# Kernel optimization log

Hardware: AMD Instinct MI355X
Metric: run time of the kernel (lower is better)

The kernel has to match this reference:

```python
import jax, jax.numpy as jnp
import numpy as np

N = 1048576   # total points across batch
C = 64        # in_planes
B = 16        # number of ragged segments (point clouds)
EPS = 1e-5


def setup_inputs() -> dict:
    key = jax.random.key(0)
    ks = jax.random.split(key, 4)
    x = jax.random.normal(ks[0], (N, C), dtype=jnp.float32)
    # cumulative end-offsets, strictly increasing, last == N
    rng = np.random.default_rng(0)
    w = rng.random(B) + 0.5
    ends = np.round(np.cumsum(w) / w.sum() * N).astype(np.int64)
    ends[-1] = N
    o = jnp.asarray(ends)
    # linear2: Linear(C, C) + ReLU (applied to per-segment mean)
    W2 = jax.random.normal(ks[1], (C, C), dtype=jnp.float32) / np.float32(np.sqrt(C))
    b2 = jnp.zeros((C,), jnp.float32)
    # linear1: BasicMLP(2C -> C): Linear + norm + ReLU
    W1 = jax.random.normal(ks[2], (2 * C, C), dtype=jnp.float32) / np.float32(np.sqrt(2 * C))
    b1 = jnp.zeros((C,), jnp.float32)
    gamma = jnp.ones((C,), jnp.float32)
    beta = jnp.zeros((C,), jnp.float32)
    return dict(x=x, o=o, W2=W2, b2=b2, W1=W1, b1=b1, gamma=gamma, beta=beta)


def reference(x, o, W2, b2, W1, b1, gamma, beta):
    n = x.shape[0]
    nseg = o.shape[0]
    # segment id of each point from cumulative offsets o
    seg = jnp.searchsorted(o, jnp.arange(n), side='right')          # [N]
    counts = jnp.diff(o, prepend=0).astype(x.dtype)                 # [B]
    # per-segment mean pool (x_b.sum(0) / cnt)
    sums = jax.ops.segment_sum(x, seg, num_segments=nseg)           # [B, C]
    means = sums / counts[:, None]
    # linear2: Linear + ReLU on the pooled vector
    xb = jax.nn.relu(means @ W2 + b2)                               # [B, C]
    # broadcast-repeat pooled feature back to points, concat with x
    h = jnp.concatenate([x, xb[seg]], axis=1)                       # [N, 2C]
    # linear1: Linear -> norm (LayerNorm stand-in for conditional norm) -> ReLU
    h = h @ W1 + b1                                                 # [N, C]
    mu = jnp.mean(h, axis=-1, keepdims=True)
    var = jnp.var(h, axis=-1, keepdims=True)
    h = (h - mu) * jax.lax.rsqrt(var + EPS) * gamma + beta
    return jax.nn.relu(h)
```

## Files before the change

kernel.cpp:

```cpp
#include <hip/hip_runtime.h>
#include <hip/hip_bf16.h>
#include <cstddef>

constexpr int C = 64;
constexpr int B = 16;

typedef __attribute__((ext_vector_type(8))) short bf16x8;
typedef __attribute__((ext_vector_type(4))) float f32x4;
typedef __attribute__((ext_vector_type(4))) unsigned int u32x4;

__device__ inline unsigned short f2bf(float f) {
    unsigned u = __builtin_bit_cast(unsigned, f);
    unsigned r = (u + 0x7FFFu + ((u >> 16) & 1u)) >> 16;
    return (unsigned short)r;
}

__device__ inline unsigned pk2(float a, float b) {
    __hip_bfloat162 t = __float22bfloat162_rn(float2{a, b});
    unsigned u;
    __builtin_memcpy(&u, &t, 4);
    return u;
}

__device__ inline bf16x8 cvt8(float4 u, float4 v) {
    u32x4 r;
    r[0] = pk2(u.x, u.y);
    r[1] = pk2(u.z, u.w);
    r[2] = pk2(v.x, v.y);
    r[3] = pk2(v.z, v.w);
    return __builtin_bit_cast(bf16x8, r);
}

__global__ __launch_bounds__(256) void seg_sum_kernel(
    const float* __restrict__ x, const int* __restrict__ o,
    float* __restrict__ sums, int N, int rows_per_block)
{
    __shared__ float lsum[B * C];
    const int tid = threadIdx.x;
    for (int i = tid; i < B * C; i += 256) lsum[i] = 0.0f;
    __syncthreads();

    const int c4 = (tid & 15) * 4;
    const int r0 = tid >> 4;
    const int row_begin = blockIdx.x * rows_per_block;
    const int row_end   = min(N, row_begin + rows_per_block);

    float ax = 0.f, ay = 0.f, az = 0.f, aw = 0.f;
    int seg = 0;
    int endcur = o[0];

    for (int r = row_begin + r0; r < row_end; r += 16) {
        while (r >= endcur) {
            if (ax != 0.f || ay != 0.f || az != 0.f || aw != 0.f) {
                atomicAdd(&lsum[seg * C + c4 + 0], ax);
                atomicAdd(&lsum[seg * C + c4 + 1], ay);
                atomicAdd(&lsum[seg * C + c4 + 2], az);
                atomicAdd(&lsum[seg * C + c4 + 3], aw);
                ax = ay = az = aw = 0.f;
            }
            ++seg;
            endcur = o[seg];
        }
        const float4 v = *reinterpret_cast<const float4*>(x + (size_t)r * C + c4);
        ax += v.x; ay += v.y; az += v.z; aw += v.w;
    }
    if (ax != 0.f || ay != 0.f || az != 0.f || aw != 0.f) {
        atomicAdd(&lsum[seg * C + c4 + 0], ax);
        atomicAdd(&lsum[seg * C + c4 + 1], ay);
        atomicAdd(&lsum[seg * C + c4 + 2], az);
        atomicAdd(&lsum[seg * C + c4 + 3], aw);
    }
    __syncthreads();

    for (int i = tid; i < B * C; i += 256) {
        const float v = lsum[i];
        if (v != 0.f) atomicAdd(&sums[i], v);
    }
}

__global__ __launch_bounds__(1024) void pooled_mlp_kernel(
    const int* __restrict__ o, const float* __restrict__ sums,
    const float* __restrict__ W2, const float* __restrict__ b2,
    const float* __restrict__ W1, const float* __restrict__ b1,
    float* __restrict__ vtab, unsigned short* __restrict__ wbf)
{
    __shared__ float means[B * C];
    __shared__ float xb[B * C];
    const int tid = threadIdx.x;
    const int b = tid >> 6;
    const int j = tid & 63;

    const int cnt = o[b] - (b ? o[b - 1] : 0);
    means[tid] = sums[tid] / (float)cnt;
    __syncthreads();

    float acc = b2[j];
#pragma unroll
    for (int c = 0; c < C; ++c)
        acc = fmaf(means[b * C + c], W2[c * C + j], acc);
    xb[tid] = fmaxf(acc, 0.f);
    __syncthreads();

    float acc2 = b1[j];
#pragma unroll
    for (int jj = 0; jj < C; ++jj)
        acc2 = fmaf(xb[b * C + jj], W1[(C + jj) * C + j], acc2);
    vtab[tid] = acc2;

    for (int idx = tid; idx < 4096; idx += 1024) {
        const int jj2 = idx & 7;
        const int ln  = (idx >> 3) & 63;
        const int tt  = (idx >> 9) & 1;
        const int ct  = idx >> 10;
        const int k   = tt * 32 + ((ln >> 4) * 8) + jj2;
        const int ch  = 4 * (ln & 15) + ct;
        wbf[idx] = f2bf(W1[k * C + ch]);
    }
}

__global__ __launch_bounds__(256) void main_mfma_kernel(
    const float* __restrict__ x, const int* __restrict__ o,
    const unsigned short* __restrict__ wbf, const float* __restrict__ vtab,
    const float* __restrict__ gamma, const float* __restrict__ beta,
    float* __restrict__ out, int N, int rows_per_wave)
{
    __shared__ float vl[B * C];
    __shared__ int osh[B];
    const int tid = threadIdx.x;
    for (int i = tid; i < B * C; i += 256) vl[i] = vtab[i];
    if (tid < B) osh[tid] = o[tid];
    __syncthreads();

    const int lane = tid & 63;
    const int wid  = tid >> 6;
    const int chb  = lane & 15;
    const int prow = (lane >> 4) * 4;

    bf16x8 wf[4][2];
#pragma unroll
    for (int ct = 0; ct < 4; ++ct)
#pragma unroll
        for (int t = 0; t < 2; ++t)
            wf[ct][t] = *reinterpret_cast<const bf16x8*>(wbf + ((ct * 2 + t) * 64 + lane) * 8);

    const float4 g4  = *reinterpret_cast<const float4*>(gamma + 4 * chb);
    const float4 bt4 = *reinterpret_cast<const float4*>(beta  + 4 * chb);

    const int gw = blockIdx.x * 4 + wid;
    const int p_begin = gw * rows_per_wave;
    if (p_begin >= N) return;
    const int p_end = min(N, p_begin + rows_per_wave);

    int seg = 0;
    while (p_begin >= osh[seg]) ++seg;
    float4 vb = *reinterpret_cast<const float4*>(vl + seg * C + 4 * chb);

    for (int p0 = p_begin; p0 < p_end; p0 += 16) {
        const float* xr = x + (size_t)(p0 + chb) * C + ((lane >> 4) * 8);
        const float4 a0 = *reinterpret_cast<const float4*>(xr);
        const float4 a1 = *reinterpret_cast<const float4*>(xr + 4);
        const float4 a2 = *reinterpret_cast<const float4*>(xr + 32);
        const float4 a3 = *reinterpret_cast<const float4*>(xr + 36);
        const bf16x8 A0 = cvt8(a0, a1);
        const bf16x8 A1 = cvt8(a2, a3);

        f32x4 acc[4];
#pragma unroll
        for (int ct = 0; ct < 4; ++ct) {
            acc[ct] = f32x4{0.f, 0.f, 0.f, 0.f};
            acc[ct] = __builtin_amdgcn_mfma_f32_16x16x32_bf16(A0, wf[ct][0], acc[ct], 0, 0, 0);
            acc[ct] = __builtin_amdgcn_mfma_f32_16x16x32_bf16(A1, wf[ct][1], acc[ct], 0, 0, 0);
        }

        float h[4][4];
        if (p0 + 16 <= osh[seg]) {
#pragma unroll
            for (int r = 0; r < 4; ++r) {
                h[0][r] = acc[0][r] + vb.x;
                h[1][r] = acc[1][r] + vb.y;
                h[2][r] = acc[2][r] + vb.z;
                h[3][r] = acc[3][r] + vb.w;
            }
        } else {
#pragma unroll
            for (int r = 0; r < 4; ++r) {
                const int p = p0 + prow + r;
                int s = seg;
                while (p >= osh[s]) ++s;
                const float4 vbs = *reinterpret_cast<const float4*>(vl + s * C + 4 * chb);
                h[0][r] = acc[0][r] + vbs.x;
                h[1][r] = acc[1][r] + vbs.y;
                h[2][r] = acc[2][r] + vbs.z;
                h[3][r] = acc[3][r] + vbs.w;
            }
        }

#pragma unroll
        for (int r = 0; r < 4; ++r) {
            float s_ = (h[0][r] + h[1][r]) + (h[2][r] + h[3][r]);
            float q_ = fmaf(h[0][r], h[0][r],
                       fmaf(h[1][r], h[1][r],
                       fmaf(h[2][r], h[2][r], h[3][r] * h[3][r])));
#pragma unroll
            for (int m = 1; m < 16; m <<= 1) {
                s_ += __shfl_xor(s_, m, 64);
                q_ += __shfl_xor(q_, m, 64);
            }
            const float mean = s_ * (1.0f / 64.0f);
            const float var  = q_ * (1.0f / 64.0f) - mean * mean;
            const float rs   = rsqrtf(var + 1e-5f);
            const int p = p0 + prow + r;

            float4 y;
            y.x = fmaxf((h[0][r] - mean) * rs * g4.x + bt4.x, 0.f);
            y.y = fmaxf((h[1][r] - mean) * rs * g4.y + bt4.y, 0.f);
            y.z = fmaxf((h[2][r] - mean) * rs * g4.z + bt4.z, 0.f);
            y.w = fmaxf((h[3][r] - mean) * rs * g4.w + bt4.w, 0.f);
            *reinterpret_cast<float4*>(out + (size_t)p * C + 4 * chb) = y;
        }

        const int pn = p0 + 16;
        if (pn < p_end && pn >= osh[seg]) {
            while (pn >= osh[seg]) ++seg;
            vb = *reinterpret_cast<const float4*>(vl + seg * C + 4 * chb);
        }
    }
}

extern "C" void kernel_launch(void* const* d_in, const int* in_sizes, int n_in,
                              void* d_out, int out_size, void* d_ws, size_t ws_size,
                              hipStream_t stream) {
    const float* x     = (const float*)d_in[0];
    const int*   o     = (const int*)d_in[1];
    const float* W2    = (const float*)d_in[2];
    const float* b2    = (const float*)d_in[3];
    const float* W1    = (const float*)d_in[4];
    const float* b1    = (const float*)d_in[5];
    const float* gamma = (const float*)d_in[6];
    const float* beta  = (const float*)d_in[7];
    float* out = (float*)d_out;

    const int N = in_sizes[0] / C;

    float* sums = (float*)d_ws;
    float* vtab = sums + B * C;
    unsigned short* wbf = (unsigned short*)(vtab + B * C);

    (void)hipMemsetAsync(sums, 0, B * C * sizeof(float), stream);

    const int rpb = 512;
    const int gridA = (N + rpb - 1) / rpb;
    seg_sum_kernel<<<gridA, 256, 0, stream>>>(x, o, sums, N, rpb);

    pooled_mlp_kernel<<<1, 1024, 0, stream>>>(o, sums, W2, b2, W1, b1, vtab, wbf);

    const int rpw = 128;
    const int nwaves = (N + rpw - 1) / rpw;
    const int gridC = (nwaves + 3) / 4;
    main_mfma_kernel<<<gridC, 256, 0, stream>>>(x, o, wbf, vtab, gamma, beta, out, N, rpw);
}
```

Measured before the change: 176.0 us.

## Fuse pooled MLP into main kernel, recompute per block, nontemporal output stores

Removes the single-block pooled_mlp kernel launch. Every block of the main kernel now recomputes the segment means, the linear2 layer, the projected pooled table and the bf16 weight fragments into shared memory. This saves one launch and its serialization gap, but adds redundant small matmuls (about 2x64x64x16 FMAs) and extra shared memory in each of 2048 blocks. Output stores also become nontemporal, to reduce cache pollution on the large streaming write.

```diff
diff --git a/kernel.cpp b/kernel.cpp
--- a/kernel.cpp
+++ b/kernel.cpp
@@ -78,57 +78,75 @@
     }
 }
 
-__global__ __launch_bounds__(1024) void pooled_mlp_kernel(
-    const int* __restrict__ o, const float* __restrict__ sums,
+__global__ __launch_bounds__(256) void main_mfma_kernel(
+    const float* __restrict__ x, const int* __restrict__ o,
+    const float* __restrict__ sums,
     const float* __restrict__ W2, const float* __restrict__ b2,
     const float* __restrict__ W1, const float* __restrict__ b1,
-    float* __restrict__ vtab, unsigned short* __restrict__ wbf)
+    const float* __restrict__ gamma, const float* __restrict__ beta,
+    float* __restrict__ out, int N, int rows_per_wave)
 {
-    __shared__ float means[B * C];
-    __shared__ float xb[B * C];
+    __shared__ float ms[B * C];
+    __shared__ float xbs[B * C];
+    __shared__ float vl[B * C];
+    __shared__ unsigned short wbfs[4096];
+    __shared__ int osh[B];
+
     const int tid = threadIdx.x;
-    const int b = tid >> 6;
+    if (tid < B) osh[tid] = o[tid];
+    __syncthreads();
+
     const int j = tid & 63;
-
-    const int cnt = o[b] - (b ? o[b - 1] : 0);
-    means[tid] = sums[tid] / (float)cnt;
-    __syncthreads();
-
-    float acc = b2[j];
-#pragma unroll
-    for (int c = 0; c < C; ++c)
-        acc = fmaf(means[b * C + c], W2[c * C + j], acc);
-    xb[tid] = fmaxf(acc, 0.f);
-    __syncthreads();
-
-    float acc2 = b1[j];
-#pragma unroll
-    for (int jj = 0; jj < C; ++jj)
-        acc2 = fmaf(xb[b * C + jj], W1[(C + jj) * C + j], acc2);
-    vtab[tid] = acc2;
-
-    for (int idx = tid; idx < 4096; idx += 1024) {
+    const int bq = tid >> 6;
+
+#pragma unroll
+    for (int q = 0; q < 4; ++q) {
+        const int b = bq * 4 + q;
+        const int cnt = osh[b] - (b ? osh[b - 1] : 0);
+        ms[b * C + j] = sums[b * C + j] / (float)cnt;
+    }
+    __syncthreads();
+
+    {
+        float acc[4];
+        const float bj = b2[j];
+#pragma unroll
+        for (int q = 0; q < 4; ++q) acc[q] = bj;
+        for (int c = 0; c < C; ++c) {
+            const float wv = W2[c * C + j];
+#pragma unroll
+            for (int q = 0; q < 4; ++q)
+                acc[q] = fmaf(ms[(bq * 4 + q) * C + c], wv, acc[q]);
+        }
+#pragma unroll
+        for (int q = 0; q < 4; ++q) xbs[(bq * 4 + q) * C + j] = fmaxf(acc[q], 0.f);
+    }
+    __syncthreads();
+
+    {
+        float acc[4];
+        const float bj = b1[j];
+#pragma unroll
+        for (int q = 0; q < 4; ++q) acc[q] = bj;
+        for (int jj = 0; jj < C; ++jj) {
+            const float wv = W1[(C + jj) * C + j];
+#pragma unroll
+            for (int q = 0; q < 4; ++q)
+                acc[q] = fmaf(xbs[(bq * 4 + q) * C + jj], wv, acc[q]);
+        }
+#pragma unroll
+        for (int q = 0; q < 4; ++q) vl[(bq * 4 + q) * C + j] = acc[q];
+    }
+
+    for (int idx = tid; idx < 4096; idx += 256) {
         const int jj2 = idx & 7;
         const int ln  = (idx >> 3) & 63;
         const int tt  = (idx >> 9) & 1;
         const int ct  = idx >> 10;
         const int k   = tt * 32 + ((ln >> 4) * 8) + jj2;
         const int ch  = 4 * (ln & 15) + ct;
-        wbf[idx] = f2bf(W1[k * C + ch]);
-    }
-}
-
-__global__ __launch_bounds__(256) void main_mfma_kernel(
-    const float* __restrict__ x, const int* __restrict__ o,
-    const unsigned short* __restrict__ wbf, const float* __restrict__ vtab,
-    const float* __restrict__ gamma, const float* __restrict__ beta,
-    float* __restrict__ out, int N, int rows_per_wave)
-{
-    __shared__ float vl[B * C];
-    __shared__ int osh[B];
-    const int tid = threadIdx.x;
-    for (int i = tid; i < B * C; i += 256) vl[i] = vtab[i];
-    if (tid < B) osh[tid] = o[tid];
+        wbfs[idx] = f2bf(W1[k * C + ch]);
+    }
     __syncthreads();
 
     const int lane = tid & 63;
@@ -141,7 +159,7 @@
     for (int ct = 0; ct < 4; ++ct)
 #pragma unroll
         for (int t = 0; t < 2; ++t)
-            wf[ct][t] = *reinterpret_cast<const bf16x8*>(wbf + ((ct * 2 + t) * 64 + lane) * 8);
+            wf[ct][t] = *reinterpret_cast<const bf16x8*>(wbfs + ((ct * 2 + t) * 64 + lane) * 8);
 
     const float4 g4  = *reinterpret_cast<const float4*>(gamma + 4 * chb);
     const float4 bt4 = *reinterpret_cast<const float4*>(beta  + 4 * chb);
@@ -211,12 +229,12 @@
             const float rs   = rsqrtf(var + 1e-5f);
             const int p = p0 + prow + r;
 
-            float4 y;
-            y.x = fmaxf((h[0][r] - mean) * rs * g4.x + bt4.x, 0.f);
-            y.y = fmaxf((h[1][r] - mean) * rs * g4.y + bt4.y, 0.f);
-            y.z = fmaxf((h[2][r] - mean) * rs * g4.z + bt4.z, 0.f);
-            y.w = fmaxf((h[3][r] - mean) * rs * g4.w + bt4.w, 0.f);
-            *reinterpret_cast<float4*>(out + (size_t)p * C + 4 * chb) = y;
+            f32x4 y;
+            y[0] = fmaxf((h[0][r] - mean) * rs * g4.x + bt4.x, 0.f);
+            y[1] = fmaxf((h[1][r] - mean) * rs * g4.y + bt4.y, 0.f);
+            y[2] = fmaxf((h[2][r] - mean) * rs * g4.z + bt4.z, 0.f);
+            y[3] = fmaxf((h[3][r] - mean) * rs * g4.w + bt4.w, 0.f);
+            __builtin_nontemporal_store(y, reinterpret_cast<f32x4*>(out + (size_t)p * C + 4 * chb));
         }
 
         const int pn = p0 + 16;
@@ -243,8 +261,6 @@
     const int N = in_sizes[0] / C;
 
     float* sums = (float*)d_ws;
-    float* vtab = sums + B * C;
-    unsigned short* wbf = (unsigned short*)(vtab + B * C);
 
     (void)hipMemsetAsync(sums, 0, B * C * sizeof(float), stream);
 
@@ -252,10 +268,9 @@
     const int gridA = (N + rpb - 1) / rpb;
     seg_sum_kernel<<<gridA, 256, 0, stream>>>(x, o, sums, N, rpb);
 
-    pooled_mlp_kernel<<<1, 1024, 0, stream>>>(o, sums, W2, b2, W1, b1, vtab, wbf);
-
     const int rpw = 128;
     const int nwaves = (N + rpw - 1) / rpw;
     const int gridC = (nwaves + 3) / 4;
-    main_mfma_kernel<<<gridC, 256, 0, stream>>>(x, o, wbf, vtab, gamma, beta, out, N, rpw);
-}
+    main_mfma_kernel<<<gridC, 256, 0, stream>>>(x, o, sums, W2, b2, W1, b1,
+                                                gamma, beta, out, N, rpw);
+}
```

Result: faster. 152.7 us (-13.2%).
